# Optimization experiments

Hardware: AMD Instinct MI355X
Metric: run time of the kernel (lower is better)

Reference implementation:

```python
import jax, jax.numpy as jnp
import numpy as np

NUM_ITEMS = 5
DIM = 1024
BATCH = 2048
NUM_PAIR = NUM_ITEMS * (NUM_ITEMS - 1)  # 20
NUM_RESULTS = 120  # 5!

# Off-diagonal ordered pairs in row-major flatten order (i*N + j, i != j).
_mask = ~np.eye(NUM_ITEMS, dtype=bool)
_IDX_I, _IDX_J = np.nonzero(_mask)  # each length NUM_PAIR
IDX_I = jnp.asarray(_IDX_I)
IDX_J = jnp.asarray(_IDX_J)


def setup_inputs() -> dict:
    key = jax.random.key(0)
    k1, k2, k3, k4, k5 = jax.random.split(key, 5)
    s_pw = 1.0 / np.sqrt(2 * DIM)
    s_cls = 1.0 / np.sqrt(NUM_PAIR * DIM)
    return {
        "embeds": jax.random.normal(k1, (BATCH, NUM_ITEMS, DIM), dtype=jnp.float32),
        "pw_w": jax.random.uniform(k2, (DIM, 2 * DIM), dtype=jnp.float32, minval=-s_pw, maxval=s_pw),
        "pw_b": jax.random.uniform(k3, (DIM,), dtype=jnp.float32, minval=-s_pw, maxval=s_pw),
        "cls_w": jax.random.uniform(k4, (NUM_RESULTS, NUM_PAIR * DIM), dtype=jnp.float32, minval=-s_cls, maxval=s_cls),
        "cls_b": jax.random.uniform(k5, (NUM_RESULTS,), dtype=jnp.float32, minval=-s_cls, maxval=s_cls),
    }


def reference(embeds, pw_w, pw_b, cls_w, cls_b):
    # Gather the two halves of each ordered off-diagonal pair directly
    # (equivalent to expand/cat/mask-select in the torch code).
    e_i = embeds[:, IDX_I, :]  # [B, P, D] : rep_1 (row item)
    e_j = embeds[:, IDX_J, :]  # [B, P, D] : rep_2 (col item)
    # pairwise_layer on concat(e_i, e_j): split weight to avoid the cat.
    w1 = pw_w[:, :DIM]
    w2 = pw_w[:, DIM:]
    pair = jnp.einsum('bpd,kd->bpk', e_i, w1) + jnp.einsum('bpd,kd->bpk', e_j, w2) + pw_b  # [B, P, D]
    flat = pair.reshape(pair.shape[0], -1)  # [B, P*D]
    return flat @ cls_w.T + cls_b  # [B, NUM_RESULTS]
```

## Files before the change

### kernel.cpp

```cpp
#include <hip/hip_runtime.h>


#define NR 120
#define KXX 5120
#define PM_SLICE (2048*128)
#define PF_SLICE (128*5120)

typedef __attribute__((ext_vector_type(8))) short bf8;
typedef __attribute__((ext_vector_type(4))) float f4;

__device__ __forceinline__ unsigned int f2bf(float f) {
    unsigned int x = __builtin_bit_cast(unsigned int, f);
    return (x + 0x7fffu + ((x >> 16) & 1u)) >> 16;
}
__device__ __forceinline__ float bf2f(unsigned short u) {
    unsigned int x = ((unsigned int)u) << 16;
    return __builtin_bit_cast(float, x);
}

__global__ __launch_bounds__(256) void k_prep(const float* __restrict__ cls_w,
                                              unsigned short* __restrict__ C2R) {
    const int col = blockIdx.x, half = blockIdx.y, t = threadIdx.x;
    const int n = col >> 7, r = col & 127;
    unsigned short* dst = C2R + (size_t)col * 2048 + half * 1024 + t * 4;
    if (r >= NR) { *(unsigned long long*)dst = 0ull; return; }
    const float* base = cls_w + (size_t)r * 20480 + t * 4;
    float sx = 0, sy = 0, sz = 0, sw = 0;
    if (half == 0) {
        #pragma unroll
        for (int q = 0; q < 4; q++) {
            float4 v = *(const float4*)(base + (4 * n + q) * 1024);
            sx += v.x; sy += v.y; sz += v.z; sw += v.w;
        }
    } else {
        #pragma unroll
        for (int i = 0; i < 5; i++) {
            if (i == n) continue;
            int q = (n > i) ? (n - 1) : n;
            float4 v = *(const float4*)(base + (4 * i + q) * 1024);
            sx += v.x; sy += v.y; sz += v.z; sw += v.w;
        }
    }
    unsigned long long pk = (unsigned long long)f2bf(sx)
                          | ((unsigned long long)f2bf(sy) << 16)
                          | ((unsigned long long)f2bf(sz) << 32)
                          | ((unsigned long long)f2bf(sw) << 48);
    *(unsigned long long*)dst = pk;
}

__global__ __launch_bounds__(256) void k_wprep(const float* __restrict__ pw_w,
                                               unsigned short* __restrict__ Afold) {
    __shared__ float T[64][65];
    const int d0 = blockIdx.x * 64, kt0 = blockIdx.y * 64;
    const int h = blockIdx.y >> 4, kr0 = (blockIdx.y & 15) * 64;
    const int t = threadIdx.x;
    #pragma unroll
    for (int lp = 0; lp < 4; lp++) {
        int lk = lp * 16 + (t >> 4);
        float4 v = *(const float4*)(pw_w + (size_t)(kr0 + lk) * 2048 + h * 1024 + d0 + (t & 15) * 4);
        T[lk][(t & 15) * 4 + 0] = v.x; T[lk][(t & 15) * 4 + 1] = v.y;
        T[lk][(t & 15) * 4 + 2] = v.z; T[lk][(t & 15) * 4 + 3] = v.w;
    }
    __syncthreads();
    #pragma unroll
    for (int wp = 0; wp < 2; wp++) {
        int ld = wp * 32 + (t >> 3);
        int lk2 = (t & 7) * 8;
        uint4 o;
        o.x = f2bf(T[lk2 + 0][ld]) | (f2bf(T[lk2 + 1][ld]) << 16);
        o.y = f2bf(T[lk2 + 2][ld]) | (f2bf(T[lk2 + 3][ld]) << 16);
        o.z = f2bf(T[lk2 + 4][ld]) | (f2bf(T[lk2 + 5][ld]) << 16);
        o.w = f2bf(T[lk2 + 6][ld]) | (f2bf(T[lk2 + 7][ld]) << 16);
        *(uint4*)(Afold + (size_t)(d0 + ld) * 2048 + kt0 + lk2) = o;
    }
}

__global__ __launch_bounds__(256) void k_const(const float* __restrict__ cls_w,
                                               const float* __restrict__ pw_b,
                                               const float* __restrict__ cls_b,
                                               float* __restrict__ constv) {
    const int r = blockIdx.x, t = threadIdx.x;
    const float* base = cls_w + (size_t)r * 20480;
    float acc = 0.f;
    for (int k = t; k < 1024; k += 256) {
        float s = 0.f;
        #pragma unroll
        for (int p = 0; p < 20; p++) s += base[p * 1024 + k];
        acc += s * pw_b[k];
    }
    __shared__ float red[256];
    red[t] = acc; __syncthreads();
    for (int s2 = 128; s2 > 0; s2 >>= 1) {
        if (t < s2) red[t] += red[t + s2];
        __syncthreads();
    }
    if (t == 0) constv[r] = cls_b[r] + red[0];
}

__global__ __launch_bounds__(256) void k_fold(const unsigned short* __restrict__ Afold,
                                              const unsigned short* __restrict__ C2R,
                                              float* __restrict__ Pf, int kchunk) {
    __shared__ __align__(16) unsigned char smem[34048];
    unsigned short* Al = (unsigned short*)smem;
    unsigned short* Bl = (unsigned short*)(smem + 8192);
    const int d0 = blockIdx.x * 64, n = blockIdx.y;
    const int kc0 = blockIdx.z * kchunk;
    const int t = threadIdx.x, lane = t & 63, wv = t >> 6;
    const int wm = wv >> 1, wn = wv & 1;
    const int rr = t >> 3, f = t & 7;

    f4 acc[2][4];
    #pragma unroll
    for (int i = 0; i < 2; i++)
        #pragma unroll
        for (int j = 0; j < 4; j++) acc[i][j] = (f4){0.f, 0.f, 0.f, 0.f};

    const unsigned short* Ag = Afold + (size_t)d0 * 2048 + kc0;
    const unsigned short* Bg = C2R + (size_t)(n * 128) * 2048 + kc0;
    uint4 ra[2], rb[4];
    #pragma unroll
    for (int p = 0; p < 2; p++)
        ra[p] = *(const uint4*)(Ag + (size_t)(p * 32 + rr) * 2048 + f * 8);
    #pragma unroll
    for (int p = 0; p < 4; p++)
        rb[p] = *(const uint4*)(Bg + (size_t)(p * 32 + rr) * 2048 + f * 8);

    const int nst = kchunk >> 6;
    for (int kt = 0; kt < nst; kt++) {
        if (kt) __syncthreads();
        #pragma unroll
        for (int p = 0; p < 2; p++) {
            int row = p * 32 + rr;
            int slot = f ^ (row & 7);
            *(uint4*)(Al + row * 64 + slot * 8) = ra[p];
        }
        #pragma unroll
        for (int p = 0; p < 4; p++) {
            int row = p * 32 + rr;
            int slot = f ^ (row & 7);
            *(uint4*)(Bl + row * 64 + slot * 8) = rb[p];
        }
        __syncthreads();
        if (kt + 1 < nst) {
            int kb = (kt + 1) * 64;
            #pragma unroll
            for (int p = 0; p < 2; p++)
                ra[p] = *(const uint4*)(Ag + (size_t)(p * 32 + rr) * 2048 + kb + f * 8);
            #pragma unroll
            for (int p = 0; p < 4; p++)
                rb[p] = *(const uint4*)(Bg + (size_t)(p * 32 + rr) * 2048 + kb + f * 8);
        }
        #pragma unroll
        for (int s = 0; s < 2; s++) {
            bf8 af[2], bq[4];
            #pragma unroll
            for (int ff = 0; ff < 2; ff++) {
                int rowa = wm * 32 + ff * 16 + (lane & 15);
                int sla = (s * 4 + (lane >> 4)) ^ (rowa & 7);
                af[ff] = *reinterpret_cast<const bf8*>(Al + rowa * 64 + sla * 8);
            }
            #pragma unroll
            for (int ff = 0; ff < 4; ff++) {
                int rowb = wn * 64 + ff * 16 + (lane & 15);
                int slb = (s * 4 + (lane >> 4)) ^ (rowb & 7);
                bq[ff] = *reinterpret_cast<const bf8*>(Bl + rowb * 64 + slb * 8);
            }
            #pragma unroll
            for (int i = 0; i < 2; i++)
                #pragma unroll
                for (int j = 0; j < 4; j++)
                    acc[i][j] = __builtin_amdgcn_mfma_f32_16x16x32_bf16(af[i], bq[j], acc[i][j], 0, 0, 0);
        }
    }
    __syncthreads();
    float* T = (float*)smem;
    #pragma unroll
    for (int i = 0; i < 2; i++) {
        int s16 = wm * 8 + i * 4 + (lane >> 4);
        #pragma unroll
        for (int j = 0; j < 4; j++) {
            int c = wn * 64 + j * 16 + (lane & 15);
            int sphy = s16 ^ (c & 15);
            *(f4*)(T + (size_t)c * 64 + sphy * 4) = acc[i][j];
        }
    }
    __syncthreads();
    float* dst = Pf + (size_t)blockIdx.z * PF_SLICE + n * 1024 + d0;
    #pragma unroll
    for (int pass = 0; pass < 4; pass++) {
        int c = pass * 32 + (t >> 3);
        #pragma unroll
        for (int u = 0; u < 2; u++) {
            int slog = (t & 7) + u * 8;
            int sphy = slog ^ (c & 15);
            float4 v = *(const float4*)(T + (size_t)c * 64 + sphy * 4);
            *(float4*)(dst + (size_t)c * KXX + slog * 4) = v;
        }
    }
}

__global__ __launch_bounds__(256) void k_foldred(const float* __restrict__ Pf,
                                                 unsigned short* __restrict__ WTt,
                                                 int ksf) {
    int i4 = blockIdx.x * 256 + threadIdx.x;
    const float4* p = (const float4*)Pf;
    float4 s = p[i4];
    for (int ks = 1; ks < ksf; ks++) {
        float4 v = p[(size_t)ks * (PF_SLICE / 4) + i4];
        s.x += v.x; s.y += v.y; s.z += v.z; s.w += v.w;
    }
    unsigned long long pk = (unsigned long long)f2bf(s.x)
                          | ((unsigned long long)f2bf(s.y) << 16)
                          | ((unsigned long long)f2bf(s.z) << 32)
                          | ((unsigned long long)f2bf(s.w) << 48);
    *(unsigned long long*)(WTt + (size_t)i4 * 4) = pk;
}

__global__ __launch_bounds__(256) void k_main(const float* __restrict__ E,
                                              const unsigned short* __restrict__ WTt,
                                              float* __restrict__ Pm, int kchunk) {
    __shared__ __align__(16) unsigned char smem[34048];
    unsigned short* Al = (unsigned short*)smem;
    unsigned short* Bl = (unsigned short*)(smem + 8192);
    const int m0 = blockIdx.x * 64;
    const int kc0 = blockIdx.y * kchunk;
    const int t = threadIdx.x, lane = t & 63, wv = t >> 6;
    const int wm = wv >> 1, wn = wv & 1;
    const int rrb = t >> 3, f = t & 7;
    const int rra = t >> 2, fa = t & 3;

    f4 acc[2][4];
    #pragma unroll
    for (int i = 0; i < 2; i++)
        #pragma unroll
        for (int j = 0; j < 4; j++) acc[i][j] = (f4){0.f, 0.f, 0.f, 0.f};

    const float* Ag = E + (size_t)m0 * KXX + kc0;
    const unsigned short* Bg = WTt + kc0;
    float4 raA[2][4];
    uint4 raB[2][4];
    const int nst = kchunk >> 6;
    #pragma unroll
    for (int st = 0; st < 2; st++) {
        int kb = st * 64;
        #pragma unroll
        for (int u = 0; u < 4; u++)
            raA[st][u] = *(const float4*)(Ag + (size_t)rra * KXX + kb + fa * 16 + u * 4);
        #pragma unroll
        for (int p = 0; p < 4; p++)
            raB[st][p] = *(const uint4*)(Bg + (size_t)(p * 32 + rrb) * KXX + kb + f * 8);
    }
    for (int kt = 0; kt < nst; kt++) {
        const int par = kt & 1;
        if (kt) __syncthreads();
        #pragma unroll
        for (int u = 0; u < 2; u++) {
            float4 v0 = raA[par][2 * u], v1 = raA[par][2 * u + 1];
            uint4 o;
            o.x = f2bf(v0.x) | (f2bf(v0.y) << 16);
            o.y = f2bf(v0.z) | (f2bf(v0.w) << 16);
            o.z = f2bf(v1.x) | (f2bf(v1.y) << 16);
            o.w = f2bf(v1.z) | (f2bf(v1.w) << 16);
            int slot = (fa * 2 + u) ^ (rra & 7);
            *(uint4*)(Al + rra * 64 + slot * 8) = o;
        }
        #pragma unroll
        for (int p = 0; p < 4; p++) {
            int row = p * 32 + rrb;
            int slot = f ^ (row & 7);
            *(uint4*)(Bl + row * 64 + slot * 8) = raB[par][p];
        }
        __syncthreads();
        if (kt + 2 < nst) {
            int kb = (kt + 2) * 64;
            #pragma unroll
            for (int u = 0; u < 4; u++)
                raA[par][u] = *(const float4*)(Ag + (size_t)rra * KXX + kb + fa * 16 + u * 4);
            #pragma unroll
            for (int p = 0; p < 4; p++)
                raB[par][p] = *(const uint4*)(Bg + (size_t)(p * 32 + rrb) * KXX + kb + f * 8);
        }
        #pragma unroll
        for (int s = 0; s < 2; s++) {
            bf8 af[2], bq[4];
            #pragma unroll
            for (int ff = 0; ff < 2; ff++) {
                int rowa = wm * 32 + ff * 16 + (lane & 15);
                int sla = (s * 4 + (lane >> 4)) ^ (rowa & 7);
                af[ff] = *reinterpret_cast<const bf8*>(Al + rowa * 64 + sla * 8);
            }
            #pragma unroll
            for (int ff = 0; ff < 4; ff++) {
                int rowb = wn * 64 + ff * 16 + (lane & 15);
                int slb = (s * 4 + (lane >> 4)) ^ (rowb & 7);
                bq[ff] = *reinterpret_cast<const bf8*>(Bl + rowb * 64 + slb * 8);
            }
            #pragma unroll
            for (int i = 0; i < 2; i++)
                #pragma unroll
                for (int j = 0; j < 4; j++)
                    acc[i][j] = __builtin_amdgcn_mfma_f32_16x16x32_bf16(af[i], bq[j], acc[i][j], 0, 0, 0);
        }
    }
    __syncthreads();
    float* T2 = (float*)smem;
    #pragma unroll
    for (int i = 0; i < 2; i++) {
        int rowb = wm * 32 + i * 16 + (lane >> 4) * 4;
        #pragma unroll
        for (int j = 0; j < 4; j++) {
            int colr = wn * 64 + j * 16 + (lane & 15);
            #pragma unroll
            for (int q = 0; q < 4; q++)
                T2[(size_t)(rowb + q) * 132 + colr] = acc[i][j][q];
        }
    }
    __syncthreads();
    float* dst = Pm + (size_t)blockIdx.y * PM_SLICE + (size_t)m0 * 128;
    {
        int row = t >> 2;
        int cb = (t & 3) * 32;
        #pragma unroll
        for (int u = 0; u < 8; u++) {
            int c = cb + u * 4;
            *(float4*)(dst + (size_t)row * 128 + c) = *(const float4*)(T2 + (size_t)row * 132 + c);
        }
    }
}

__global__ __launch_bounds__(256) void k_mainred(const float* __restrict__ Pm,
                                                 const float* __restrict__ constv,
                                                 float* __restrict__ out, int nksm) {
    int tid = blockIdx.x * 256 + threadIdx.x;
    int b = tid / NR, r = tid - b * NR;
    float s = constv[r];
    for (int ks = 0; ks < nksm; ks++)
        s += Pm[(size_t)ks * PM_SLICE + (size_t)b * 128 + r];
    out[tid] = s;
}

extern "C" void kernel_launch(void* const* d_in, const int* in_sizes, int n_in,
                              void* d_out, int out_size, void* d_ws, size_t ws_size,
                              hipStream_t stream) {
    const float* embeds = (const float*)d_in[0];
    const float* pw_w   = (const float*)d_in[1];
    const float* pw_b   = (const float*)d_in[2];
    const float* cls_w  = (const float*)d_in[3];
    const float* cls_b  = (const float*)d_in[4];
    float* out = (float*)d_out;

    unsigned short* C2R   = (unsigned short*)d_ws;
    unsigned short* Afold = C2R + (size_t)640 * 2048;
    unsigned short* WTt   = Afold + (size_t)1024 * 2048;
    float* constv = (float*)(WTt + (size_t)128 * 5120);
    float* scratch = constv + 128;

    size_t base = ((size_t)640 * 2048 + (size_t)1024 * 2048 + (size_t)128 * 5120) * 2 + 512;
    size_t avail = (ws_size > base) ? (ws_size - base) / 4 : 0;
    const int candm[5] = {16, 8, 4, 2, 1};
    int nksm = 1;
    for (int ci = 0; ci < 5; ci++)
        if ((size_t)candm[ci] * PM_SLICE <= avail) { nksm = candm[ci]; break; }
    const int candf[4] = {8, 4, 2, 1};
    int ksf = 1;
    for (int ci = 0; ci < 4; ci++)
        if ((size_t)candf[ci] * PF_SLICE <= avail) { ksf = candf[ci]; break; }

    k_const<<<dim3(NR), dim3(256), 0, stream>>>(cls_w, pw_b, cls_b, constv);
    k_prep<<<dim3(640, 2), dim3(256), 0, stream>>>(cls_w, C2R);
    k_wprep<<<dim3(16, 32), dim3(256), 0, stream>>>(pw_w, Afold);
    k_fold<<<dim3(16, 5, ksf), dim3(256), 0, stream>>>(Afold, C2R, scratch, 2048 / ksf);
    k_foldred<<<dim3(640), dim3(256), 0, stream>>>(scratch, WTt, ksf);
    k_main<<<dim3(32, nksm), dim3(256), 0, stream>>>(embeds, WTt, scratch, KXX / nksm);
    k_mainred<<<dim3(960), dim3(256), 0, stream>>>(scratch, constv, out, nksm);
}
```

Measured before the change: 179.7 us.

## Write MFMA fragments directly to split-K scratch and remap in reduction kernels

Result: slower. 233.0 us (+29.7%).

```diff
diff --git a/kernel.cpp b/kernel.cpp
--- a/kernel.cpp
+++ b/kernel.cpp
@@ -12,10 +12,6 @@
 __device__ __forceinline__ unsigned int f2bf(float f) {
     unsigned int x = __builtin_bit_cast(unsigned int, f);
     return (x + 0x7fffu + ((x >> 16) & 1u)) >> 16;
-}
-__device__ __forceinline__ float bf2f(unsigned short u) {
-    unsigned int x = ((unsigned int)u) << 16;
-    return __builtin_bit_cast(float, x);
 }
 
 __global__ __launch_bounds__(256) void k_prep(const float* __restrict__ cls_w,
@@ -100,9 +96,9 @@
 __global__ __launch_bounds__(256) void k_fold(const unsigned short* __restrict__ Afold,
                                               const unsigned short* __restrict__ C2R,
                                               float* __restrict__ Pf, int kchunk) {
-    __shared__ __align__(16) unsigned char smem[34048];
-    unsigned short* Al = (unsigned short*)smem;
-    unsigned short* Bl = (unsigned short*)(smem + 8192);
+    __shared__ __align__(16) unsigned short lds[(64 + 128) * 64];
+    unsigned short* Al = lds;
+    unsigned short* Bl = lds + 64 * 64;
     const int d0 = blockIdx.x * 64, n = blockIdx.y;
     const int kc0 = blockIdx.z * kchunk;
     const int t = threadIdx.x, lane = t & 63, wv = t >> 6;
@@ -172,56 +168,46 @@
                     acc[i][j] = __builtin_amdgcn_mfma_f32_16x16x32_bf16(af[i], bq[j], acc[i][j], 0, 0, 0);
         }
     }
-    __syncthreads();
-    float* T = (float*)smem;
-    #pragma unroll
-    for (int i = 0; i < 2; i++) {
-        int s16 = wm * 8 + i * 4 + (lane >> 4);
-        #pragma unroll
-        for (int j = 0; j < 4; j++) {
-            int c = wn * 64 + j * 16 + (lane & 15);
-            int sphy = s16 ^ (c & 15);
-            *(f4*)(T + (size_t)c * 64 + sphy * 4) = acc[i][j];
-        }
-    }
-    __syncthreads();
-    float* dst = Pf + (size_t)blockIdx.z * PF_SLICE + n * 1024 + d0;
-    #pragma unroll
-    for (int pass = 0; pass < 4; pass++) {
-        int c = pass * 32 + (t >> 3);
-        #pragma unroll
-        for (int u = 0; u < 2; u++) {
-            int slog = (t & 7) + u * 8;
-            int sphy = slog ^ (c & 15);
-            float4 v = *(const float4*)(T + (size_t)c * 64 + sphy * 4);
-            *(float4*)(dst + (size_t)c * KXX + slog * 4) = v;
-        }
-    }
+    float* dst = Pf + (size_t)blockIdx.z * PF_SLICE
+               + ((size_t)(blockIdx.x * 5 + n)) * 8192;
+    #pragma unroll
+    for (int i = 0; i < 2; i++)
+        #pragma unroll
+        for (int j = 0; j < 4; j++)
+            *(f4*)(dst + (((i * 4 + j) * 256 + t) * 4)) = acc[i][j];
 }
 
 __global__ __launch_bounds__(256) void k_foldred(const float* __restrict__ Pf,
                                                  unsigned short* __restrict__ WTt,
                                                  int ksf) {
-    int i4 = blockIdx.x * 256 + threadIdx.x;
-    const float4* p = (const float4*)Pf;
-    float4 s = p[i4];
+    int tid = blockIdx.x * 256 + threadIdx.x;
+    int r = tid / 1280, x4 = tid - r * 1280;
+    int n = x4 >> 8;
+    int dtile = (x4 & 255) >> 4;
+    int wm = (x4 & 15) >> 3;
+    int i = (x4 >> 2) & 1;
+    int lanehi = x4 & 3;
+    int wn = r >> 6, j = (r >> 4) & 3, lanelo = r & 15;
+    int tsrc = (wm * 2 + wn) * 64 + lanehi * 16 + lanelo;
+    size_t idx = ((((size_t)(dtile * 5 + n) * 2 + i) * 4 + j) * 256 + tsrc) * 4;
+    float4 s = *(const float4*)(Pf + idx);
     for (int ks = 1; ks < ksf; ks++) {
-        float4 v = p[(size_t)ks * (PF_SLICE / 4) + i4];
+        float4 v = *(const float4*)(Pf + (size_t)ks * PF_SLICE + idx);
         s.x += v.x; s.y += v.y; s.z += v.z; s.w += v.w;
     }
     unsigned long long pk = (unsigned long long)f2bf(s.x)
                           | ((unsigned long long)f2bf(s.y) << 16)
                           | ((unsigned long long)f2bf(s.z) << 32)
                           | ((unsigned long long)f2bf(s.w) << 48);
-    *(unsigned long long*)(WTt + (size_t)i4 * 4) = pk;
+    *(unsigned long long*)(WTt + (size_t)r * KXX + x4 * 4) = pk;
 }
 
 __global__ __launch_bounds__(256) void k_main(const float* __restrict__ E,
                                               const unsigned short* __restrict__ WTt,
                                               float* __restrict__ Pm, int kchunk) {
-    __shared__ __align__(16) unsigned char smem[34048];
-    unsigned short* Al = (unsigned short*)smem;
-    unsigned short* Bl = (unsigned short*)(smem + 8192);
+    __shared__ __align__(16) unsigned short lds[(64 + 128) * 64];
+    unsigned short* Al = lds;
+    unsigned short* Bl = lds + 64 * 64;
     const int m0 = blockIdx.x * 64;
     const int kc0 = blockIdx.y * kchunk;
     const int t = threadIdx.x, lane = t & 63, wv = t >> 6;
@@ -302,41 +288,37 @@
                     acc[i][j] = __builtin_amdgcn_mfma_f32_16x16x32_bf16(af[i], bq[j], acc[i][j], 0, 0, 0);
         }
     }
-    __syncthreads();
-    float* T2 = (float*)smem;
-    #pragma unroll
-    for (int i = 0; i < 2; i++) {
-        int rowb = wm * 32 + i * 16 + (lane >> 4) * 4;
-        #pragma unroll
-        for (int j = 0; j < 4; j++) {
-            int colr = wn * 64 + j * 16 + (lane & 15);
-            #pragma unroll
-            for (int q = 0; q < 4; q++)
-                T2[(size_t)(rowb + q) * 132 + colr] = acc[i][j][q];
-        }
-    }
-    __syncthreads();
-    float* dst = Pm + (size_t)blockIdx.y * PM_SLICE + (size_t)m0 * 128;
-    {
-        int row = t >> 2;
-        int cb = (t & 3) * 32;
-        #pragma unroll
-        for (int u = 0; u < 8; u++) {
-            int c = cb + u * 4;
-            *(float4*)(dst + (size_t)row * 128 + c) = *(const float4*)(T2 + (size_t)row * 132 + c);
-        }
-    }
+    float* dst = Pm + (size_t)blockIdx.y * PM_SLICE + (size_t)blockIdx.x * 8192;
+    #pragma unroll
+    for (int i = 0; i < 2; i++)
+        #pragma unroll
+        for (int j = 0; j < 4; j++)
+            *(f4*)(dst + (((i * 4 + j) * 256 + t) * 4)) = acc[i][j];
 }
 
 __global__ __launch_bounds__(256) void k_mainred(const float* __restrict__ Pm,
                                                  const float* __restrict__ constv,
                                                  float* __restrict__ out, int nksm) {
     int tid = blockIdx.x * 256 + threadIdx.x;
-    int b = tid / NR, r = tid - b * NR;
-    float s = constv[r];
-    for (int ks = 0; ks < nksm; ks++)
-        s += Pm[(size_t)ks * PM_SLICE + (size_t)b * 128 + r];
-    out[tid] = s;
+    int b4 = tid / NR, r = tid - b4 * NR;
+    int mtile = b4 >> 4;
+    int wm = (b4 & 15) >> 3;
+    int i = (b4 >> 2) & 1;
+    int lanehi = b4 & 3;
+    int wn = r >> 6, j = (r >> 4) & 3, lanelo = r & 15;
+    int tsrc = (wm * 2 + wn) * 64 + lanehi * 16 + lanelo;
+    size_t idx = (((size_t)(mtile * 2 + i) * 4 + j) * 256 + tsrc) * 4;
+    float4 s = *(const float4*)(Pm + idx);
+    for (int ks = 1; ks < nksm; ks++) {
+        float4 v = *(const float4*)(Pm + (size_t)ks * PM_SLICE + idx);
+        s.x += v.x; s.y += v.y; s.z += v.z; s.w += v.w;
+    }
+    float c = constv[r];
+    int b = b4 * 4;
+    out[(size_t)(b + 0) * NR + r] = s.x + c;
+    out[(size_t)(b + 1) * NR + r] = s.y + c;
+    out[(size_t)(b + 2) * NR + r] = s.z + c;
+    out[(size_t)(b + 3) * NR + r] = s.w + c;
 }
 
 extern "C" void kernel_launch(void* const* d_in, const int* in_sizes, int n_in,
@@ -357,13 +339,13 @@
 
     size_t base = ((size_t)640 * 2048 + (size_t)1024 * 2048 + (size_t)128 * 5120) * 2 + 512;
     size_t avail = (ws_size > base) ? (ws_size - base) / 4 : 0;
-    const int candm[5] = {16, 8, 4, 2, 1};
+    const int candm[9] = {40, 20, 16, 10, 8, 5, 4, 2, 1};
     int nksm = 1;
+    for (int ci = 0; ci < 9; ci++)
+        if ((size_t)candm[ci] * PM_SLICE <= avail) { nksm = candm[ci]; break; }
+    const int candf[5] = {16, 8, 4, 2, 1};
+    int ksf = 1;
     for (int ci = 0; ci < 5; ci++)
-        if ((size_t)candm[ci] * PM_SLICE <= avail) { nksm = candm[ci]; break; }
-    const int candf[4] = {8, 4, 2, 1};
-    int ksf = 1;
-    for (int ci = 0; ci < 4; ci++)
         if ((size_t)candf[ci] * PF_SLICE <= avail) { ksf = candf[ci]; break; }
 
     k_const<<<dim3(NR), dim3(256), 0, stream>>>(cls_w, pw_b, cls_b, constv);
@@ -372,5 +354,5 @@
     k_fold<<<dim3(16, 5, ksf), dim3(256), 0, stream>>>(Afold, C2R, scratch, 2048 / ksf);
     k_foldred<<<dim3(640), dim3(256), 0, stream>>>(scratch, WTt, ksf);
     k_main<<<dim3(32, nksm), dim3(256), 0, stream>>>(embeds, WTt, scratch, KXX / nksm);
-    k_mainred<<<dim3(960), dim3(256), 0, stream>>>(scratch, constv, out, nksm);
-}
+    k_mainred<<<dim3(240), dim3(256), 0, stream>>>(scratch, constv, out, nksm);
+}
```
